# Kernel optimization log

Hardware: AMD Instinct MI355X
Metric: run time of the kernel (lower is better)

Reference implementation:

```python
import jax, jax.numpy as jnp
import numpy as np

N_NODES = 100000


def gcn_conv(x, edge_index, W, b):
    """PyG GCNConv: add self-loops, symmetric deg^-1/2 normalization, linear."""
    n = x.shape[0]
    h = x @ W  # [N, out]
    loop = jnp.arange(n, dtype=edge_index.dtype)
    src = jnp.concatenate([edge_index[0], loop])
    dst = jnp.concatenate([edge_index[1], loop])
    deg = jax.ops.segment_sum(jnp.ones_like(dst, dtype=h.dtype), dst, num_segments=n)
    dinv = jnp.where(deg > 0, jax.lax.rsqrt(deg), 0.0)
    norm = dinv[src] * dinv[dst]  # [E+N]
    msg = h[src] * norm[:, None]  # gather + scale
    out = jax.ops.segment_sum(msg, dst, num_segments=n)  # scatter-add
    return out + b


def setup_inputs() -> dict:
    key = jax.random.key(0)
    k1, k2, k3, k4 = jax.random.split(key, 4)
    d_in, d_hid, d_out = 128, 128, 128  # output_dim // 2 = 128
    E = 1600000
    x = jax.random.normal(k1, (N_NODES, d_in), dtype=jnp.float32)
    edge_index = jax.random.randint(k2, (2, E), 0, N_NODES, dtype=jnp.int64)
    s1 = 1.0 / np.sqrt(d_in)
    s2 = 1.0 / np.sqrt(d_hid)
    W1 = jax.random.normal(k3, (d_in, d_hid), dtype=jnp.float32) * s1
    b1 = jnp.zeros((d_hid,), dtype=jnp.float32)
    W2 = jax.random.normal(k4, (d_hid, d_out), dtype=jnp.float32) * s2
    b2 = jnp.zeros((d_out,), dtype=jnp.float32)
    return {"x": x, "edge_index": edge_index, "W1": W1, "b1": b1, "W2": W2, "b2": b2}


def reference(x, edge_index, W1, b1, W2, b2):
    h = jax.nn.relu(gcn_conv(x, edge_index, W1, b1))
    # dropout(p=0.5) is identity in eval mode
    return gcn_conv(h, edge_index, W2, b2)
```

## Files before the change

### kernel.cpp

```cpp
#include <hip/hip_runtime.h>

#define D 128

typedef unsigned int uint;
typedef unsigned short ushort;
typedef __attribute__((ext_vector_type(8))) short bf16x8_t;
typedef __attribute__((ext_vector_type(4))) float f32x4_t;

#define BSH 9
#define BMASK 511
#define BN 512
#define CAP 9216
#define CHUNK 8192
#define NBUCKP 256

__global__ __launch_bounds__(256) void kp_scatter3(const int* __restrict__ src,
                                                   const int* __restrict__ dst,
                                                   int* __restrict__ gcnt,
                                                   uint* __restrict__ bkt, int E, int nbuck) {
    __shared__ uint stage[CHUNK];
    __shared__ int cnt[NBUCKP], loc[NBUCKP], cnt2[NBUCKP], gbase[NBUCKP];
    int t = threadIdx.x;
    int base = blockIdx.x * CHUNK;
    int end = min(E, base + CHUNK);

    cnt[t] = 0; cnt2[t] = 0; gbase[t] = 0;
    __syncthreads();
    for (int i = base + t; i < end; i += 256)
        atomicAdd(&cnt[dst[i] >> BSH], 1);
    __syncthreads();
    int v = cnt[t];
    loc[t] = v;
    __syncthreads();
    for (int off = 1; off < NBUCKP; off <<= 1) {
        int x = (t >= off) ? loc[t - off] : 0;
        __syncthreads();
        loc[t] += x;
        __syncthreads();
    }
    if (t < nbuck && cnt[t] > 0)
        gbase[t] = atomicAdd(&gcnt[t], cnt[t]);
    __syncthreads();
    for (int i = base + t; i < end; i += 256) {
        int d = dst[i], s = src[i];
        int bk = d >> BSH;
        int r = atomicAdd(&cnt2[bk], 1);
        stage[(loc[bk] - cnt[bk]) + r] = ((uint)s << BSH) | (uint)(d & BMASK);
    }
    __syncthreads();
    int wave = t >> 6, lane = t & 63;
    for (int bk = wave; bk < nbuck; bk += 4) {
        int c = cnt[bk];
        if (c == 0) continue;
        int lo = loc[bk] - c;
        int gb = gbase[bk];
        uint* ob = bkt + (size_t)bk * CAP;
        for (int j = lane; j < c; j += 64) {
            int di = gb + j;
            if (di < CAP) ob[di] = stage[lo + j];
        }
    }
}

__global__ __launch_bounds__(256) void kp_build3(uint* __restrict__ bkt,
                                                 const int* __restrict__ gcnt,
                                                 int* __restrict__ row_start,
                                                 int* __restrict__ row_end,
                                                 float* __restrict__ dinv, int n) {
    __shared__ uint ents[CAP];
    __shared__ int cnt[BN], loc[BN], cnt2[BN];
    int t = threadIdx.x, b = blockIdx.x;
    int m = gcnt[b];
    if (m > CAP) m = CAP;
    uint* bk = bkt + (size_t)b * CAP;
    for (int i = t; i < m; i += 256) ents[i] = bk[i];
    cnt[t] = 0; cnt[t + 256] = 0; cnt2[t] = 0; cnt2[t + 256] = 0;
    __syncthreads();
    for (int i = t; i < m; i += 256) atomicAdd(&cnt[ents[i] & BMASK], 1);
    __syncthreads();
    int i0 = t, i1 = t + 256;
    int v0 = cnt[i0], v1 = cnt[i1];
    loc[i0] = v0; loc[i1] = v1;
    __syncthreads();
    for (int off = 1; off < BN; off <<= 1) {
        int x0 = (i0 >= off) ? loc[i0 - off] : 0;
        int x1 = (i1 >= off) ? loc[i1 - off] : 0;
        __syncthreads();
        loc[i0] += x0; loc[i1] += x1;
        __syncthreads();
    }
    int base = b * CAP;
    int node0 = (b << BSH) + i0, node1 = (b << BSH) + i1;
    if (node0 < n) {
        row_start[node0] = base + loc[i0] - v0;
        row_end[node0]   = base + loc[i0];
        dinv[node0] = rsqrtf((float)(v0 + 1));
    }
    if (node1 < n) {
        row_start[node1] = base + loc[i1] - v1;
        row_end[node1]   = base + loc[i1];
        dinv[node1] = rsqrtf((float)(v1 + 1));
    }
    __syncthreads();
    for (int i = t; i < m; i += 256) {
        uint p = ents[i];
        int low = p & BMASK;
        int r = atomicAdd(&cnt2[low], 1);
        ((int*)bk)[(loc[low] - cnt[low]) + r] = (int)((p >> BSH) << 8);
    }
}

__device__ inline uint bf16rn(float f) {
    uint u = __float_as_uint(f);
    return (u + 0x7fffu + ((u >> 16) & 1u)) >> 16;
}

__device__ inline void accum_bf16x8(float* a, uint4 v) {
    a[0] += __uint_as_float(v.x << 16);
    a[1] += __uint_as_float(v.x & 0xffff0000u);
    a[2] += __uint_as_float(v.y << 16);
    a[3] += __uint_as_float(v.y & 0xffff0000u);
    a[4] += __uint_as_float(v.z << 16);
    a[5] += __uint_as_float(v.z & 0xffff0000u);
    a[6] += __uint_as_float(v.w << 16);
    a[7] += __uint_as_float(v.w & 0xffff0000u);
}

__global__ void k_prep_w2(const float* __restrict__ W1, const float* __restrict__ W2,
                          ushort* __restrict__ W1h, ushort* __restrict__ W1l,
                          ushort* __restrict__ W2h, ushort* __restrict__ W2l) {
    int i = blockIdx.x * blockDim.x + threadIdx.x;
    int sel = i >> 14;
    int j = i & 16383;
    int k = j >> 7, nn = j & 127;
    const float* W = sel ? W2 : W1;
    float w = W[k * D + nn];
    uint hb = bf16rn(w);
    float hf = __uint_as_float(hb << 16);
    uint lb = bf16rn(w - hf);
    if (sel) { W2h[nn * D + k] = (ushort)hb; W2l[nn * D + k] = (ushort)lb; }
    else     { W1h[nn * D + k] = (ushort)hb; W1l[nn * D + k] = (ushort)lb; }
}

template <bool A_FP32>
__global__ __launch_bounds__(256, 2) void k_gemm_mfma(const void* __restrict__ A,
                                                      const ushort* __restrict__ Wth,
                                                      const ushort* __restrict__ Wtl,
                                                      const float* __restrict__ dinv,
                                                      ushort* __restrict__ Yb, int M) {
    constexpr int STR = 72;
    constexpr int TILE = 128 * STR;
    __shared__ ushort lds[A_FP32 ? 4 * TILE : 3 * TILE];
    ushort* Ah = lds;
    ushort* Wh = lds + TILE;
    ushort* Wl = lds + 2 * TILE;
    ushort* Al = A_FP32 ? (lds + 3 * TILE) : nullptr;

    int t = threadIdx.x;
    int lane = t & 63, wave = t >> 6;
    int quad = lane >> 4, l16 = lane & 15;
    int m_off = (wave & 1) * 64;
    int n_off = (wave >> 1) * 64;
    int block_row = blockIdx.x * 128;

    f32x4_t acc[4][4];
#pragma unroll
    for (int mt = 0; mt < 4; mt++)
#pragma unroll
        for (int nt = 0; nt < 4; nt++) acc[mt][nt] = (f32x4_t){0.f, 0.f, 0.f, 0.f};

    for (int kc = 0; kc < 128; kc += 64) {
        if (A_FP32) {
            const float* Af = (const float*)A;
#pragma unroll
            for (int it = 0; it < 8; it++) {
                int s = t + it * 256;
                int row = s >> 4, kl = (s & 15) * 4;
                int gr = block_row + row;
                float4 v = make_float4(0.f, 0.f, 0.f, 0.f);
                if (gr < M) v = *(const float4*)(Af + (size_t)gr * D + kc + kl);
                ushort4 h, l;
                uint hb, lb; float hf;
                hb = bf16rn(v.x); hf = __uint_as_float(hb << 16); lb = bf16rn(v.x - hf);
                h.x = (ushort)hb; l.x = (ushort)lb;
                hb = bf16rn(v.y); hf = __uint_as_float(hb << 16); lb = bf16rn(v.y - hf);
                h.y = (ushort)hb; l.y = (ushort)lb;
                hb = bf16rn(v.z); hf = __uint_as_float(hb << 16); lb = bf16rn(v.z - hf);
                h.z = (ushort)hb; l.z = (ushort)lb;
                hb = bf16rn(v.w); hf = __uint_as_float(hb << 16); lb = bf16rn(v.w - hf);
                h.w = (ushort)hb; l.w = (ushort)lb;
                *(ushort4*)&Ah[row * STR + kl] = h;
                *(ushort4*)&Al[row * STR + kl] = l;
            }
        } else {
            const ushort* Ab = (const ushort*)A;
#pragma unroll
            for (int it = 0; it < 4; it++) {
                int s = t + it * 256;
                int row = s >> 3, kl = (s & 7) * 8;
                int gr = block_row + row;
                uint4 v = make_uint4(0u, 0u, 0u, 0u);
                if (gr < M) v = *(const uint4*)(Ab + (size_t)gr * D + kc + kl);
                *(uint4*)&Ah[row * STR + kl] = v;
            }
        }
#pragma unroll
        for (int it = 0; it < 4; it++) {
            int s = t + it * 256;
            int nrow = s >> 3, kl = (s & 7) * 8;
            *(uint4*)&Wh[nrow * STR + kl] = *(const uint4*)(Wth + nrow * D + kc + kl);
            *(uint4*)&Wl[nrow * STR + kl] = *(const uint4*)(Wtl + nrow * D + kc + kl);
        }
        __syncthreads();

#pragma unroll
        for (int ks = 0; ks < 2; ks++) {
            int kf = ks * 32 + quad * 8;
            bf16x8_t ah[4], bh[4], bl[4];
#pragma unroll
            for (int mt = 0; mt < 4; mt++)
                ah[mt] = *(const bf16x8_t*)&Ah[(m_off + mt * 16 + l16) * STR + kf];
#pragma unroll
            for (int nt = 0; nt < 4; nt++) {
                bh[nt] = *(const bf16x8_t*)&Wh[(n_off + nt * 16 + l16) * STR + kf];
                bl[nt] = *(const bf16x8_t*)&Wl[(n_off + nt * 16 + l16) * STR + kf];
            }
            if (A_FP32) {
                bf16x8_t al[4];
#pragma unroll
                for (int mt = 0; mt < 4; mt++)
                    al[mt] = *(const bf16x8_t*)&Al[(m_off + mt * 16 + l16) * STR + kf];
#pragma unroll
                for (int mt = 0; mt < 4; mt++)
#pragma unroll
                    for (int nt = 0; nt < 4; nt++) {
                        acc[mt][nt] = __builtin_amdgcn_mfma_f32_16x16x32_bf16(ah[mt], bh[nt], acc[mt][nt], 0, 0, 0);
                        acc[mt][nt] = __builtin_amdgcn_mfma_f32_16x16x32_bf16(al[mt], bh[nt], acc[mt][nt], 0, 0, 0);
                        acc[mt][nt] = __builtin_amdgcn_mfma_f32_16x16x32_bf16(ah[mt], bl[nt], acc[mt][nt], 0, 0, 0);
                    }
            } else {
#pragma unroll
                for (int mt = 0; mt < 4; mt++)
#pragma unroll
                    for (int nt = 0; nt < 4; nt++) {
                        acc[mt][nt] = __builtin_amdgcn_mfma_f32_16x16x32_bf16(ah[mt], bh[nt], acc[mt][nt], 0, 0, 0);
                        acc[mt][nt] = __builtin_amdgcn_mfma_f32_16x16x32_bf16(ah[mt], bl[nt], acc[mt][nt], 0, 0, 0);
                    }
            }
        }
        __syncthreads();
    }

#pragma unroll
    for (int mt = 0; mt < 4; mt++) {
#pragma unroll
        for (int reg = 0; reg < 4; reg++) {
            int gr = block_row + m_off + mt * 16 + quad * 4 + reg;
            if (gr < M) {
                float di = dinv[gr];
#pragma unroll
                for (int nt = 0; nt < 4; nt++) {
                    int colg = n_off + nt * 16 + l16;
                    Yb[(size_t)gr * D + colg] = (ushort)bf16rn(di * acc[mt][nt][reg]);
                }
            }
        }
    }
}

__global__ __launch_bounds__(256) void k_agg(const ushort* __restrict__ Hb,
                                             const int* __restrict__ row_start,
                                             const int* __restrict__ row_end,
                                             const int* __restrict__ colb,
                                             const float* __restrict__ dinv,
                                             const float* __restrict__ bias,
                                             float* __restrict__ Yf, ushort* __restrict__ Yb,
                                             int n, int do_relu, int out_bf16) {
    __shared__ int ls[4][64];
    int wv = threadIdx.x >> 6;
    int node = blockIdx.x * 4 + wv;
    int lane = threadIdx.x & 63;
    int chain = lane >> 4;
    int l16   = lane & 15;
    if (node >= n) return;

    int start = row_start[node];
    int end   = row_end[node];

    float a0[8], a1[8];
#pragma unroll
    for (int k = 0; k < 8; k++) { a0[k] = 0.f; a1[k] = 0.f; }

    const char* hbase = (const char*)Hb;
    uint loff = (uint)l16 * 16u;

    if (chain == 0) {
        uint4 v = *(const uint4*)(hbase + (uint)node * 256u + loff);
        accum_bf16x8(a0, v);
    }

    for (int tb = start; tb < end; tb += 64) {
        int idx = tb + lane;
        ls[wv][lane] = (idx < end) ? colb[idx] : 0;
        int c = min(64, end - tb);
        int j = chain;
        for (; j + 12 < c; j += 16) {
            uint o0 = (uint)ls[wv][j];
            uint o1 = (uint)ls[wv][j + 4];
            uint o2 = (uint)ls[wv][j + 8];
            uint o3 = (uint)ls[wv][j + 12];
            uint4 v0 = *(const uint4*)(hbase + o0 + loff);
            uint4 v1 = *(const uint4*)(hbase + o1 + loff);
            uint4 v2 = *(const uint4*)(hbase + o2 + loff);
            uint4 v3 = *(const uint4*)(hbase + o3 + loff);
            accum_bf16x8(a0, v0);
            accum_bf16x8(a1, v1);
            accum_bf16x8(a0, v2);
            accum_bf16x8(a1, v3);
        }
        for (; j + 4 < c; j += 8) {
            uint o0 = (uint)ls[wv][j];
            uint o1 = (uint)ls[wv][j + 4];
            uint4 v0 = *(const uint4*)(hbase + o0 + loff);
            uint4 v1 = *(const uint4*)(hbase + o1 + loff);
            accum_bf16x8(a0, v0);
            accum_bf16x8(a1, v1);
        }
        if (j < c) {
            uint o0 = (uint)ls[wv][j];
            uint4 v0 = *(const uint4*)(hbase + o0 + loff);
            accum_bf16x8(a0, v0);
        }
    }

    float acc[8];
#pragma unroll
    for (int k = 0; k < 8; k++) {
        float v = a0[k] + a1[k];
        v += __shfl_xor(v, 16, 64);
        v += __shfl_xor(v, 32, 64);
        acc[k] = v;
    }

    if (chain == 0) {
        float di = dinv[node];
        const float4* bp = (const float4*)bias + l16 * 2;
        float4 b0 = bp[0], b1 = bp[1];
        float o[8];
        o[0] = fmaf(di, acc[0], b0.x); o[1] = fmaf(di, acc[1], b0.y);
        o[2] = fmaf(di, acc[2], b0.z); o[3] = fmaf(di, acc[3], b0.w);
        o[4] = fmaf(di, acc[4], b1.x); o[5] = fmaf(di, acc[5], b1.y);
        o[6] = fmaf(di, acc[6], b1.z); o[7] = fmaf(di, acc[7], b1.w);
        if (do_relu) {
#pragma unroll
            for (int k = 0; k < 8; k++) o[k] = fmaxf(o[k], 0.f);
        }
        if (out_bf16) {
            uint4 pk;
            pk.x = bf16rn(o[0]) | (bf16rn(o[1]) << 16);
            pk.y = bf16rn(o[2]) | (bf16rn(o[3]) << 16);
            pk.z = bf16rn(o[4]) | (bf16rn(o[5]) << 16);
            pk.w = bf16rn(o[6]) | (bf16rn(o[7]) << 16);
            ((uint4*)(Yb + (size_t)node * D))[l16] = pk;
        } else {
            f32x4_t q0 = {o[0], o[1], o[2], o[3]};
            f32x4_t q1 = {o[4], o[5], o[6], o[7]};
            f32x4_t* yp = (f32x4_t*)(Yf + (size_t)node * D) + l16 * 2;
            __builtin_nontemporal_store(q0, yp);
            __builtin_nontemporal_store(q1, yp + 1);
        }
    }
}

extern "C" void kernel_launch(void* const* d_in, const int* in_sizes, int n_in,
                              void* d_out, int out_size, void* d_ws, size_t ws_size,
                              hipStream_t stream) {
    const float* x  = (const float*)d_in[0];
    const int*   ei = (const int*)d_in[1];
    const float* W1 = (const float*)d_in[2];
    const float* b1 = (const float*)d_in[3];
    const float* W2 = (const float*)d_in[4];
    const float* b2 = (const float*)d_in[5];
    float* out = (float*)d_out;

    int n = in_sizes[0] / D;
    int E = in_sizes[1] / 2;
    const int* src = ei;
    const int* dst = ei + E;

    int nbuck = (n + BMASK) >> BSH;

    char* p = (char*)d_ws;
    ushort* h_buf = (ushort*)p; p += (size_t)n * D * sizeof(ushort);
    ushort* y_buf = (ushort*)p; p += (size_t)n * D * sizeof(ushort);
    ushort* w1h   = (ushort*)p; p += (size_t)D * D * sizeof(ushort);
    ushort* w1l   = (ushort*)p; p += (size_t)D * D * sizeof(ushort);
    ushort* w2h   = (ushort*)p; p += (size_t)D * D * sizeof(ushort);
    ushort* w2l   = (ushort*)p; p += (size_t)D * D * sizeof(ushort);
    uint*  bkt    = (uint*)p;   p += (size_t)nbuck * CAP * sizeof(uint);
    float* dinv   = (float*)p;  p += (size_t)n * sizeof(float);
    int*   row_s  = (int*)p;    p += (size_t)n * sizeof(int);
    int*   row_e  = (int*)p;    p += (size_t)n * sizeof(int);
    int*   gcnt   = (int*)p;    p += (size_t)nbuck * sizeof(int);

    (void)hipMemsetAsync(gcnt, 0, (size_t)nbuck * sizeof(int), stream);
    int sc_grid = (E + CHUNK - 1) / CHUNK;
    kp_scatter3<<<sc_grid, 256, 0, stream>>>(src, dst, gcnt, bkt, E, nbuck);
    kp_build3<<<nbuck, 256, 0, stream>>>(bkt, gcnt, row_s, row_e, dinv, n);

    k_prep_w2<<<128, 256, 0, stream>>>(W1, W2, w1h, w1l, w2h, w2l);

    int gemm_grid = (n + 127) / 128;
    int agg_grid  = (n + 3) / 4;
    const int* colp = (const int*)bkt;

    k_gemm_mfma<true><<<gemm_grid, 256, 0, stream>>>(x, w1h, w1l, dinv, h_buf, n);
    k_agg<<<agg_grid, 256, 0, stream>>>(h_buf, row_s, row_e, colp, dinv, b1, nullptr, y_buf, n, 1, 1);
    k_gemm_mfma<false><<<gemm_grid, 256, 0, stream>>>(y_buf, w2h, w2l, dinv, h_buf, n);
    k_agg<<<agg_grid, 256, 0, stream>>>(h_buf, row_s, row_e, colp, dinv, b2, out, nullptr, n, 0, 0);
}
```

Baseline: 337.5 us.

## Fuse weight prep into build kernel, pack row bounds, shrink scatter chunks

The weight split/transpose kernel is folded into the CSR build kernel as extra blocks, which removes one launch. The build kernel now uses 512 threads, one per node in a bucket. Row start and end are packed into one int2 so the aggregation kernel does a single load per node. The scatter chunk size drops from 8192 to 2048 edges, with 16-thread groups writing out each bucket, to get more blocks and better parallelism. The trade-off is more global atomics on bucket counts and smaller coalesced write segments.

```diff
diff --git a/kernel.cpp b/kernel.cpp
--- a/kernel.cpp
+++ b/kernel.cpp
@@ -11,8 +11,13 @@
 #define BMASK 511
 #define BN 512
 #define CAP 9216
-#define CHUNK 8192
+#define CHUNK 2048
 #define NBUCKP 256
+
+__device__ inline uint bf16rn(float f) {
+    uint u = __float_as_uint(f);
+    return (u + 0x7fffu + ((u >> 16) & 1u)) >> 16;
+}
 
 __global__ __launch_bounds__(256) void kp_scatter3(const int* __restrict__ src,
                                                    const int* __restrict__ dst,
@@ -48,71 +53,75 @@
         stage[(loc[bk] - cnt[bk]) + r] = ((uint)s << BSH) | (uint)(d & BMASK);
     }
     __syncthreads();
-    int wave = t >> 6, lane = t & 63;
-    for (int bk = wave; bk < nbuck; bk += 4) {
+    int grp = t >> 4, gl = t & 15;
+    for (int bk = grp; bk < nbuck; bk += 16) {
         int c = cnt[bk];
         if (c == 0) continue;
         int lo = loc[bk] - c;
         int gb = gbase[bk];
         uint* ob = bkt + (size_t)bk * CAP;
-        for (int j = lane; j < c; j += 64) {
+        for (int j = gl; j < c; j += 16) {
             int di = gb + j;
             if (di < CAP) ob[di] = stage[lo + j];
         }
     }
 }
 
-__global__ __launch_bounds__(256) void kp_build3(uint* __restrict__ bkt,
+__global__ __launch_bounds__(512) void kp_build3(uint* __restrict__ bkt,
                                                  const int* __restrict__ gcnt,
-                                                 int* __restrict__ row_start,
-                                                 int* __restrict__ row_end,
-                                                 float* __restrict__ dinv, int n) {
+                                                 int2* __restrict__ row_se,
+                                                 float* __restrict__ dinv, int n, int nbuck,
+                                                 const float* __restrict__ W1,
+                                                 const float* __restrict__ W2,
+                                                 ushort* __restrict__ W1h, ushort* __restrict__ W1l,
+                                                 ushort* __restrict__ W2h, ushort* __restrict__ W2l) {
+    int t = threadIdx.x, b = blockIdx.x;
+    if (b >= nbuck) {
+        int i = (b - nbuck) * 512 + t;
+        int sel = i >> 14;
+        int j = i & 16383;
+        int k = j >> 7, nn = j & 127;
+        const float* W = sel ? W2 : W1;
+        float w = W[k * D + nn];
+        uint hb = bf16rn(w);
+        float hf = __uint_as_float(hb << 16);
+        uint lb = bf16rn(w - hf);
+        if (sel) { W2h[nn * D + k] = (ushort)hb; W2l[nn * D + k] = (ushort)lb; }
+        else     { W1h[nn * D + k] = (ushort)hb; W1l[nn * D + k] = (ushort)lb; }
+        return;
+    }
     __shared__ uint ents[CAP];
     __shared__ int cnt[BN], loc[BN], cnt2[BN];
-    int t = threadIdx.x, b = blockIdx.x;
     int m = gcnt[b];
     if (m > CAP) m = CAP;
     uint* bk = bkt + (size_t)b * CAP;
-    for (int i = t; i < m; i += 256) ents[i] = bk[i];
-    cnt[t] = 0; cnt[t + 256] = 0; cnt2[t] = 0; cnt2[t + 256] = 0;
-    __syncthreads();
-    for (int i = t; i < m; i += 256) atomicAdd(&cnt[ents[i] & BMASK], 1);
-    __syncthreads();
-    int i0 = t, i1 = t + 256;
-    int v0 = cnt[i0], v1 = cnt[i1];
-    loc[i0] = v0; loc[i1] = v1;
+    for (int i = t; i < m; i += 512) ents[i] = bk[i];
+    cnt[t] = 0; cnt2[t] = 0;
+    __syncthreads();
+    for (int i = t; i < m; i += 512) atomicAdd(&cnt[ents[i] & BMASK], 1);
+    __syncthreads();
+    int v = cnt[t];
+    loc[t] = v;
     __syncthreads();
     for (int off = 1; off < BN; off <<= 1) {
-        int x0 = (i0 >= off) ? loc[i0 - off] : 0;
-        int x1 = (i1 >= off) ? loc[i1 - off] : 0;
-        __syncthreads();
-        loc[i0] += x0; loc[i1] += x1;
+        int x = (t >= off) ? loc[t - off] : 0;
+        __syncthreads();
+        loc[t] += x;
         __syncthreads();
     }
     int base = b * CAP;
-    int node0 = (b << BSH) + i0, node1 = (b << BSH) + i1;
-    if (node0 < n) {
-        row_start[node0] = base + loc[i0] - v0;
-        row_end[node0]   = base + loc[i0];
-        dinv[node0] = rsqrtf((float)(v0 + 1));
-    }
-    if (node1 < n) {
-        row_start[node1] = base + loc[i1] - v1;
-        row_end[node1]   = base + loc[i1];
-        dinv[node1] = rsqrtf((float)(v1 + 1));
-    }
-    __syncthreads();
-    for (int i = t; i < m; i += 256) {
+    int node = (b << BSH) + t;
+    if (node < n) {
+        row_se[node] = make_int2(base + loc[t] - v, base + loc[t]);
+        dinv[node] = rsqrtf((float)(v + 1));
+    }
+    __syncthreads();
+    for (int i = t; i < m; i += 512) {
         uint p = ents[i];
         int low = p & BMASK;
         int r = atomicAdd(&cnt2[low], 1);
         ((int*)bk)[(loc[low] - cnt[low]) + r] = (int)((p >> BSH) << 8);
     }
-}
-
-__device__ inline uint bf16rn(float f) {
-    uint u = __float_as_uint(f);
-    return (u + 0x7fffu + ((u >> 16) & 1u)) >> 16;
 }
 
 __device__ inline void accum_bf16x8(float* a, uint4 v) {
@@ -124,22 +133,6 @@
     a[5] += __uint_as_float(v.z & 0xffff0000u);
     a[6] += __uint_as_float(v.w << 16);
     a[7] += __uint_as_float(v.w & 0xffff0000u);
-}
-
-__global__ void k_prep_w2(const float* __restrict__ W1, const float* __restrict__ W2,
-                          ushort* __restrict__ W1h, ushort* __restrict__ W1l,
-                          ushort* __restrict__ W2h, ushort* __restrict__ W2l) {
-    int i = blockIdx.x * blockDim.x + threadIdx.x;
-    int sel = i >> 14;
-    int j = i & 16383;
-    int k = j >> 7, nn = j & 127;
-    const float* W = sel ? W2 : W1;
-    float w = W[k * D + nn];
-    uint hb = bf16rn(w);
-    float hf = __uint_as_float(hb << 16);
-    uint lb = bf16rn(w - hf);
-    if (sel) { W2h[nn * D + k] = (ushort)hb; W2l[nn * D + k] = (ushort)lb; }
-    else     { W1h[nn * D + k] = (ushort)hb; W1l[nn * D + k] = (ushort)lb; }
 }
 
 template <bool A_FP32>
@@ -269,8 +262,7 @@
 }
 
 __global__ __launch_bounds__(256) void k_agg(const ushort* __restrict__ Hb,
-                                             const int* __restrict__ row_start,
-                                             const int* __restrict__ row_end,
+                                             const int2* __restrict__ row_se,
                                              const int* __restrict__ colb,
                                              const float* __restrict__ dinv,
                                              const float* __restrict__ bias,
@@ -284,8 +276,8 @@
     int l16   = lane & 15;
     if (node >= n) return;
 
-    int start = row_start[node];
-    int end   = row_end[node];
+    int2 se = row_se[node];
+    int start = se.x, end = se.y;
 
     float a0[8], a1[8];
 #pragma unroll
@@ -399,23 +391,21 @@
     ushort* w2l   = (ushort*)p; p += (size_t)D * D * sizeof(ushort);
     uint*  bkt    = (uint*)p;   p += (size_t)nbuck * CAP * sizeof(uint);
     float* dinv   = (float*)p;  p += (size_t)n * sizeof(float);
-    int*   row_s  = (int*)p;    p += (size_t)n * sizeof(int);
-    int*   row_e  = (int*)p;    p += (size_t)n * sizeof(int);
+    int2*  row_se = (int2*)p;   p += (size_t)n * sizeof(int2);
     int*   gcnt   = (int*)p;    p += (size_t)nbuck * sizeof(int);
 
     (void)hipMemsetAsync(gcnt, 0, (size_t)nbuck * sizeof(int), stream);
     int sc_grid = (E + CHUNK - 1) / CHUNK;
     kp_scatter3<<<sc_grid, 256, 0, stream>>>(src, dst, gcnt, bkt, E, nbuck);
-    kp_build3<<<nbuck, 256, 0, stream>>>(bkt, gcnt, row_s, row_e, dinv, n);
-
-    k_prep_w2<<<128, 256, 0, stream>>>(W1, W2, w1h, w1l, w2h, w2l);
+    kp_build3<<<nbuck + 64, 512, 0, stream>>>(bkt, gcnt, row_se, dinv, n, nbuck,
+                                              W1, W2, w1h, w1l, w2h, w2l);
 
     int gemm_grid = (n + 127) / 128;
     int agg_grid  = (n + 3) / 4;
     const int* colp = (const int*)bkt;
 
     k_gemm_mfma<true><<<gemm_grid, 256, 0, stream>>>(x, w1h, w1l, dinv, h_buf, n);
-    k_agg<<<agg_grid, 256, 0, stream>>>(h_buf, row_s, row_e, colp, dinv, b1, nullptr, y_buf, n, 1, 1);
+    k_agg<<<agg_grid, 256, 0, stream>>>(h_buf, row_se, colp, dinv, b1, nullptr, y_buf, n, 1, 1);
     k_gemm_mfma<false><<<gemm_grid, 256, 0, stream>>>(y_buf, w2h, w2l, dinv, h_buf, n);
-    k_agg<<<agg_grid, 256, 0, stream>>>(h_buf, row_s, row_e, colp, dinv, b2, out, nullptr, n, 0, 0);
-}
+    k_agg<<<agg_grid, 256, 0, stream>>>(h_buf, row_se, colp, dinv, b2, out, nullptr, n, 0, 0);
+}
```

After: 325.5 us. -3.5%, faster.
